# Performance work log

Hardware: AMD Instinct MI355X
Metric: run time of the kernel (lower is better)

The kernel has to match this reference:

```python
import jax, jax.numpy as jnp
import numpy as np

N_EMBD = 2048
QKV_EMBD = 2048
N_HEAD = 32
N_KV_HEAD = 8
HEAD_DIM = QKV_EMBD // N_HEAD  # 64
GROUPS = N_HEAD // N_KV_HEAD   # 4
ROPE_THETA = 10000.0
SCALE = float(np.sqrt(HEAD_DIM))


def setup_inputs() -> dict:
    key = jax.random.key(0)
    ks = jax.random.split(key, 12)
    B, S = 2, 2048
    inp = {
        "query": jax.random.normal(ks[0], (B, S, N_EMBD), jnp.float32),
        "key": jax.random.normal(ks[1], (B, S, N_EMBD), jnp.float32),
        "value": jax.random.normal(ks[2], (B, S, N_EMBD), jnp.float32),
        "mask": jnp.ones((B, S), dtype=bool),
        "Wq": jax.random.normal(ks[3], (QKV_EMBD, N_EMBD), jnp.float32) * 0.02,
        "bq": jnp.zeros((QKV_EMBD,), jnp.float32),
        "Wk": jax.random.normal(ks[4], (N_KV_HEAD * HEAD_DIM, N_EMBD), jnp.float32) * 0.02,
        "bk": jnp.zeros((N_KV_HEAD * HEAD_DIM,), jnp.float32),
        "Wv": jax.random.normal(ks[5], (N_KV_HEAD * HEAD_DIM, N_EMBD), jnp.float32) * 0.02,
        "bv": jnp.zeros((N_KV_HEAD * HEAD_DIM,), jnp.float32),
        "Wo": jax.random.normal(ks[6], (N_EMBD, QKV_EMBD), jnp.float32) * 0.02,
        "bo": jnp.zeros((N_EMBD,), jnp.float32),
    }
    return inp


def _rotate_half(x):
    d = x.shape[-1] // 2
    return jnp.concatenate([-x[..., d:], x[..., :d]], axis=-1)


def _rope_cos_sin(seq_len, dtype):
    # rope_factor == 1.0 -> no NTK adjustment; is_causal -> position_ids = arange
    inv_freq = 1.0 / (ROPE_THETA ** (jnp.arange(0, HEAD_DIM, 2, dtype=jnp.float32) / HEAD_DIM))
    pos = jnp.arange(seq_len, dtype=jnp.float32)
    freqs = jnp.einsum("i,j->ij", pos, inv_freq)           # [S, D/2]
    emb = jnp.concatenate([freqs, freqs], axis=-1)          # [S, D]
    return jnp.cos(emb).astype(dtype)[None, None], jnp.sin(emb).astype(dtype)[None, None]


def reference(query, key, value, mask, Wq, bq, Wk, bk, Wv, bv, Wo, bo):
    B, S, _ = query.shape
    Q = (query @ Wq.T + bq).reshape(B, S, N_HEAD, HEAD_DIM).transpose(0, 2, 1, 3)      # [B,H,S,D]
    K = (key @ Wk.T + bk).reshape(B, S, N_KV_HEAD, HEAD_DIM).transpose(0, 2, 1, 3)     # [B,KV,S,D]
    V = (value @ Wv.T + bv).reshape(B, S, N_KV_HEAD, HEAD_DIM).transpose(0, 2, 1, 3)

    cos, sin = _rope_cos_sin(S, Q.dtype)
    Q = Q * cos + _rotate_half(Q) * sin
    K = K * cos + _rotate_half(K) * sin

    # interleaved GQA repeat: each kv head serves GROUPS consecutive query heads
    K = jnp.repeat(K, GROUPS, axis=1)  # [B,H,S,D]
    V = jnp.repeat(V, GROUPS, axis=1)

    attn = jnp.einsum("bhqd,bhkd->bhqk", Q, K)              # [B,H,S,S]
    causal = jnp.tril(jnp.ones((S, S), dtype=bool))
    full_mask = mask[:, None, None, :] & causal[None, None]  # [B,1,S,S]
    attn = jnp.where(full_mask, attn, jnp.finfo(attn.dtype).min)
    attn_weights = jax.nn.softmax(attn / SCALE, axis=-1)     # dropout p=0 (eval)
    out = jnp.einsum("bhqk,bhkd->bhqd", attn_weights, V)
    out = out.transpose(0, 2, 1, 3).reshape(B, S, QKV_EMBD)
    return out @ Wo.T + bo
```

## Files before the change

kernel.cpp:

```cpp
#include <hip/hip_runtime.h>
#include <hip/hip_bf16.h>
#include <cmath>

#define NE   2048
#define NH   32
#define NKV  8
#define HD   64
#define SEQ  2048
#define NB   2

typedef __attribute__((ext_vector_type(4))) float f32x4;
typedef __attribute__((ext_vector_type(16))) float f32x16;
typedef __attribute__((ext_vector_type(8))) short bf16x8;
typedef __attribute__((ext_vector_type(4))) short bf16x4;
typedef __attribute__((ext_vector_type(4))) unsigned u32x4;

typedef const __attribute__((address_space(1))) void cgvoid;
typedef __attribute__((address_space(3))) void lvoid;

#define QSCALE 0.18033688011112042f

__device__ __forceinline__ short f2bf(float f) {
  union { float f; unsigned u; } v; v.f = f;
  unsigned r = v.u + 0x7fffu + ((v.u >> 16) & 1u);
  return (short)(r >> 16);
}

__device__ __forceinline__ unsigned cvt_pk_bf16(float a, float b) {
  unsigned r;
  asm("v_cvt_pk_bf16_f32 %0, %1, %2" : "=v"(r) : "v"(a), "v"(b));
  return r;
}

__global__ __launch_bounds__(256) void cvt_w(
    const float* __restrict__ s0, short* __restrict__ d0,
    const float* __restrict__ s1, short* __restrict__ d1,
    const float* __restrict__ s2, short* __restrict__ d2,
    const float* __restrict__ s3, short* __restrict__ d3)
{
  int idx = blockIdx.x * 256 + threadIdx.x;
  const float* s; short* d; int rel;
  if      (idx < 524288)  { s = s0; d = d0; rel = idx; }
  else if (idx < 655360)  { s = s1; d = d1; rel = idx - 524288; }
  else if (idx < 786432)  { s = s2; d = d2; rel = idx - 655360; }
  else                    { s = s3; d = d3; rel = idx - 786432; }
  size_t off = (size_t)rel * 8;
  f32x4 a = *(const f32x4*)(s + off);
  f32x4 b = *(const f32x4*)(s + off + 4);
  bf16x8 o;
  #pragma unroll
  for (int j = 0; j < 4; ++j) { o[j] = f2bf(a[j]); o[4 + j] = f2bf(b[j]); }
  *(bf16x8*)(d + off) = o;
}

template<int EPI>
__device__ __forceinline__ void gemm256_body(
    short* As, short* Ws, int m0, int n0,
    const float* __restrict__ A, const short* __restrict__ W,
    const float* __restrict__ bias, void* __restrict__ Cout, int K)
{
  const int t = threadIdx.x, lane = t & 63, w = t >> 6;
  const int lr = lane & 15, lg = lane >> 4;
  const int wm = (w >> 2) * 128, wn = (w & 3) * 64;

  f32x4 acc[8][4];
  #pragma unroll
  for (int i = 0; i < 8; ++i)
    #pragma unroll
    for (int j = 0; j < 4; ++j) acc[i][j] = (f32x4){0.f, 0.f, 0.f, 0.f};

  auto STAGE_W = [&](int kt) {
    const int k0 = kt << 6;
    short* Wd = Ws + (kt & 1) * 16384;
    #pragma unroll
    for (int it = 0; it < 4; ++it) {
      int e = it * 512 + t, r = e >> 3, c = e & 7;
      int cs = ((c ^ (r & 7)) << 3);
      __builtin_amdgcn_global_load_lds((cgvoid*)(W + (size_t)(n0 + r) * K + k0 + cs),
                                       (lvoid*)(Wd + e * 8), 16, 0, 0);
    }
  };

  f32x4 areg[4][2];
  auto LOAD_A = [&](int kt) {
    const int k0 = kt << 6;
    #pragma unroll
    for (int it = 0; it < 4; ++it) {
      int e = it * 512 + t, r = e >> 3, c = e & 7;
      int cs = ((c ^ (r & 7)) << 3);
      const float* src = A + (size_t)(m0 + r) * K + k0 + cs;
      areg[it][0] = *(const f32x4*)(src);
      areg[it][1] = *(const f32x4*)(src + 4);
    }
  };
  auto WRITE_A = [&](int kt) {
    short* Ad = As + (kt & 1) * 16384;
    #pragma unroll
    for (int it = 0; it < 4; ++it) {
      int e = it * 512 + t;
      u32x4 v;
      v[0] = cvt_pk_bf16(areg[it][0][0], areg[it][0][1]);
      v[1] = cvt_pk_bf16(areg[it][0][2], areg[it][0][3]);
      v[2] = cvt_pk_bf16(areg[it][1][0], areg[it][1][1]);
      v[3] = cvt_pk_bf16(areg[it][1][2], areg[it][1][3]);
      *(u32x4*)(Ad + e * 8) = v;
    }
  };

  const int nt = K >> 6;

  LOAD_A(0);
  STAGE_W(0);
  WRITE_A(0);
  asm volatile("s_waitcnt lgkmcnt(0)" ::: "memory");

  #pragma unroll 1
  for (int ti = 0; ti < nt; ++ti) {
    const short* Ab = As + (ti & 1) * 16384;
    const short* Wb = Ws + (ti & 1) * 16384;
    if (ti + 1 < nt) {
      LOAD_A(ti + 1);
      STAGE_W(ti + 1);
      asm volatile("s_waitcnt vmcnt(12)" ::: "memory");
    } else {
      asm volatile("s_waitcnt vmcnt(0)" ::: "memory");
    }
    __builtin_amdgcn_s_barrier();

    bf16x8 wf[2][4];
    #pragma unroll
    for (int ks = 0; ks < 2; ++ks)
      #pragma unroll
      for (int nf = 0; nf < 4; ++nf) {
        int row = wn + nf * 16 + lr;
        wf[ks][nf] = *(const bf16x8*)(Wb + row * 64 + (((ks * 4 + lg) ^ (row & 7)) << 3));
      }
    #pragma unroll
    for (int mq = 0; mq < 4; ++mq) {
      bf16x8 af[2][2];
      #pragma unroll
      for (int ks = 0; ks < 2; ++ks)
        #pragma unroll
        for (int mi = 0; mi < 2; ++mi) {
          int row = wm + (mq * 2 + mi) * 16 + lr;
          af[ks][mi] = *(const bf16x8*)(Ab + row * 64 + (((ks * 4 + lg) ^ (row & 7)) << 3));
        }
      __builtin_amdgcn_s_setprio(1);
      #pragma unroll
      for (int ks = 0; ks < 2; ++ks)
        #pragma unroll
        for (int mi = 0; mi < 2; ++mi)
          #pragma unroll
          for (int nf = 0; nf < 4; ++nf)
            acc[mq * 2 + mi][nf] =
                __builtin_amdgcn_mfma_f32_16x16x32_bf16(af[ks][mi], wf[ks][nf],
                                                        acc[mq * 2 + mi][nf], 0, 0, 0);
      __builtin_amdgcn_s_setprio(0);
    }
    if (ti + 1 < nt) WRITE_A(ti + 1);
    asm volatile("s_waitcnt lgkmcnt(0)" ::: "memory");
    __builtin_amdgcn_s_barrier();
  }

  if (EPI == 1) {
    short* C = (short*)Cout;
    #pragma unroll
    for (int mf = 0; mf < 8; ++mf)
      #pragma unroll
      for (int nf = 0; nf < 4; ++nf) {
        int n = n0 + wn + nf * 16 + lr;
        int kv = n >> 6, d = n & 63;
        int mb = m0 + wm + mf * 16 + lg * 4;
        int b = mb >> 11, s = mb & (SEQ - 1);
        bf16x4 pb;
        #pragma unroll
        for (int i = 0; i < 4; ++i) pb[i] = f2bf(acc[mf][nf][i] + bias[n]);
        *(bf16x4*)(C + (((size_t)b * NKV + kv) * HD + d) * SEQ + s) = pb;
      }
  } else {
    const int HN = (EPI == 2) ? NH : NKV;
    short* C = (short*)Cout;
    #pragma unroll
    for (int mf = 0; mf < 8; ++mf)
      #pragma unroll
      for (int nf2 = 0; nf2 < 2; ++nf2) {
        int n1 = n0 + wn + nf2 * 16 + lr;
        int d1 = n1 & 63;
        int h = n1 >> 6;
        float inv = exp2f(-(float)d1 * (13.287712379549449f / 32.0f));
        #pragma unroll
        for (int i = 0; i < 4; ++i) {
          int m = m0 + wm + mf * 16 + lg * 4 + i;
          int b = m >> 11, s = m & (SEQ - 1);
          float v1 = acc[mf][nf2][i] + bias[n1];
          float v2 = acc[mf][nf2 + 2][i] + bias[n1 + 32];
          float ang = (float)s * inv;
          float c, sn;
          __sincosf(ang, &sn, &c);
          float o1 = v1 * c - v2 * sn;
          float o2 = v2 * c + v1 * sn;
          if (EPI == 2) { o1 *= QSCALE; o2 *= QSCALE; }
          size_t base = (((size_t)b * HN + h) * SEQ + s) * HD;
          C[base + d1]      = f2bf(o1);
          C[base + d1 + 32] = f2bf(o2);
        }
      }
  }
}

__global__ __launch_bounds__(512, 2) void gemm_qkv256(
    const float* __restrict__ qA, const short* __restrict__ Wq,
    const float* __restrict__ bq, short* __restrict__ Qout,
    const float* __restrict__ kA, const short* __restrict__ Wk,
    const float* __restrict__ bk, short* __restrict__ Kout,
    const float* __restrict__ vA, const short* __restrict__ Wv,
    const float* __restrict__ bv, short* __restrict__ Vout)
{
  __shared__ __align__(16) short As[2 * 256 * 64];
  __shared__ __align__(16) short Ws[2 * 256 * 64];
  int orig = blockIdx.x;
  int xcd = orig & 7, idx = orig >> 3;
  int hiP = (idx >= 12) ? 1 : 0;
  int mm = xcd + 8 * hiP;
  int j = idx - 12 * hiP;
  if (j < 8) {
    gemm256_body<2>(As, Ws, mm * 256, j * 256, qA, Wq, bq, (void*)Qout, NE);
  } else if (j < 10) {
    gemm256_body<3>(As, Ws, mm * 256, (j - 8) * 256, kA, Wk, bk, (void*)Kout, NE);
  } else {
    gemm256_body<1>(As, Ws, mm * 256, (j - 10) * 256, vA, Wv, bv, (void*)Vout, NE);
  }
}

__global__ __launch_bounds__(256) void gemm_o(
    const short* __restrict__ A, const short* __restrict__ W,
    const float* __restrict__ bias, float* __restrict__ C, int N, int K)
{
  __shared__ __align__(16) short As[2 * 128 * 64];
  __shared__ __align__(16) short Ws[2 * 128 * 64];
  const int t = threadIdx.x, lane = t & 63, w = t >> 6;
  const int lr = lane & 15, lg = lane >> 4;
  const int wm = (w >> 1) * 64, wn = (w & 1) * 64;
  const int L = blockIdx.x;
  const int xcd = L & 7, slot = L >> 3;
  const int bx = xcd + 8 * (slot >> 4);
  const int byy = slot & 15;
  const int m0 = bx * 128, n0 = byy * 128;

  f32x4 acc[4][4];
  #pragma unroll
  for (int i = 0; i < 4; ++i)
    #pragma unroll
    for (int j = 0; j < 4; ++j) acc[i][j] = (f32x4){0.f, 0.f, 0.f, 0.f};

  const int nt = K >> 6;
  #pragma unroll
  for (int it = 0; it < 4; ++it) {
    int e = it * 256 + t, r = e >> 3, c = e & 7;
    int cs = ((c ^ (r & 7)) << 3);
    __builtin_amdgcn_global_load_lds((cgvoid*)(A + (size_t)(m0 + r) * K + cs),
                                     (lvoid*)(As + e * 8), 16, 0, 0);
    __builtin_amdgcn_global_load_lds((cgvoid*)(W + (size_t)(n0 + r) * K + cs),
                                     (lvoid*)(Ws + e * 8), 16, 0, 0);
  }

  for (int ti = 0; ti < nt; ++ti) {
    const int cur = ti & 1;
    const short* Ab = As + cur * 8192;
    const short* Wb = Ws + cur * 8192;
    if (ti + 1 < nt) {
      const int k0 = (ti + 1) << 6;
      short* An = As + (cur ^ 1) * 8192;
      short* Wn = Ws + (cur ^ 1) * 8192;
      #pragma unroll
      for (int it = 0; it < 4; ++it) {
        int e = it * 256 + t, r = e >> 3, c = e & 7;
        int cs = ((c ^ (r & 7)) << 3);
        __builtin_amdgcn_global_load_lds((cgvoid*)(A + (size_t)(m0 + r) * K + k0 + cs),
                                         (lvoid*)(An + e * 8), 16, 0, 0);
        __builtin_amdgcn_global_load_lds((cgvoid*)(W + (size_t)(n0 + r) * K + k0 + cs),
                                         (lvoid*)(Wn + e * 8), 16, 0, 0);
      }
      asm volatile("s_waitcnt vmcnt(8)" ::: "memory");
    } else {
      asm volatile("s_waitcnt vmcnt(0)" ::: "memory");
    }
    __builtin_amdgcn_s_barrier();
    __builtin_amdgcn_sched_barrier(0);

    bf16x8 wf[2][4];
    #pragma unroll
    for (int ks = 0; ks < 2; ++ks)
      #pragma unroll
      for (int nf = 0; nf < 4; ++nf) {
        int row = wn + nf * 16 + lr;
        wf[ks][nf] = *(const bf16x8*)(Wb + row * 64 + (((ks * 4 + lg) ^ (row & 7)) << 3));
      }
    #pragma unroll
    for (int mq = 0; mq < 2; ++mq) {
      bf16x8 af[2][2];
      #pragma unroll
      for (int ks = 0; ks < 2; ++ks)
        #pragma unroll
        for (int mi = 0; mi < 2; ++mi) {
          int row = wm + (mq * 2 + mi) * 16 + lr;
          af[ks][mi] = *(const bf16x8*)(Ab + row * 64 + (((ks * 4 + lg) ^ (row & 7)) << 3));
        }
      __builtin_amdgcn_s_setprio(1);
      #pragma unroll
      for (int ks = 0; ks < 2; ++ks)
        #pragma unroll
        for (int mi = 0; mi < 2; ++mi)
          #pragma unroll
          for (int nf = 0; nf < 4; ++nf)
            acc[mq * 2 + mi][nf] =
                __builtin_amdgcn_mfma_f32_16x16x32_bf16(af[ks][mi], wf[ks][nf],
                                                        acc[mq * 2 + mi][nf], 0, 0, 0);
      __builtin_amdgcn_s_setprio(0);
      __builtin_amdgcn_s_barrier();
      __builtin_amdgcn_sched_barrier(0);
    }
  }

  #pragma unroll
  for (int mf = 0; mf < 4; ++mf)
    #pragma unroll
    for (int nf = 0; nf < 4; ++nf)
      #pragma unroll
      for (int i = 0; i < 4; ++i) {
        int m = m0 + wm + mf * 16 + lg * 4 + i;
        int n = n0 + wn + nf * 16 + lr;
        C[(size_t)m * N + n] = acc[mf][nf][i] + bias[n];
      }
}

__global__ __launch_bounds__(256) void attn_kernel(
    const short* __restrict__ Q, const short* __restrict__ K,
    const short* __restrict__ Vt, short* __restrict__ O)
{
  __shared__ __align__(16) short Ks[2][64 * 64];
  __shared__ __align__(16) short Vs[2][64 * 64];

  const int t = threadIdx.x, lane = t & 63, w = t >> 6;
  const int l31 = lane & 31, hi = lane >> 5;
  const int L = blockIdx.x;
  const int xcd = L & 7, slot = L >> 3;
  const int by = xcd + 8 * (slot >> 5);
  const int bx = slot & 31;
  const int b = by >> 3, kvh = by & 7;
  const int h = kvh * 4 + w;

  const short* Qh = Q + ((size_t)b * NH + h) * SEQ * HD;
  const short* Kh = K + ((size_t)b * NKV + kvh) * SEQ * HD;
  const short* Vh = Vt + ((size_t)b * NKV + kvh) * (size_t)HD * SEQ;

  #pragma unroll 1
  for (int pass = 0; pass < 2; ++pass) {
    const int qb32 = pass ? bx : (63 - bx);
    const int q0 = qb32 * 32;
    const int ntile = (qb32 >> 1) + 1;
    const int qpos = q0 + l31;

    bf16x8 qfr[4];
    #pragma unroll
    for (int dd = 0; dd < 4; ++dd)
      qfr[dd] = *(const bf16x8*)(Qh + (size_t)(q0 + l31) * HD + dd * 16 + hi * 8);

    f32x16 o[2];
    #pragma unroll
    for (int dh = 0; dh < 2; ++dh)
      #pragma unroll
      for (int r = 0; r < 16; ++r) o[dh][r] = 0.f;
    float lsum = 0.f;

    #pragma unroll
    for (int it = 0; it < 2; ++it) {
      int cid = it * 256 + t;
      int r = cid >> 3, c = cid & 7;
      int cs = ((c ^ (r & 7)) << 3);
      __builtin_amdgcn_global_load_lds((cgvoid*)(Kh + (size_t)r * HD + cs),
                                       (lvoid*)(Ks[0] + cid * 8), 16, 0, 0);
      __builtin_amdgcn_global_load_lds((cgvoid*)(Vh + (size_t)r * SEQ + cs),
                                       (lvoid*)(Vs[0] + cid * 8), 16, 0, 0);
    }
    __syncthreads();

    for (int ti = 0; ti < ntile; ++ti) {
      const int cur = ti & 1;
      if (ti + 1 < ntile) {
        const int kvn = (ti + 1) * 64;
        #pragma unroll
        for (int it = 0; it < 2; ++it) {
          int cid = it * 256 + t;
          int r = cid >> 3, c = cid & 7;
          int cs = ((c ^ (r & 7)) << 3);
          __builtin_amdgcn_global_load_lds((cgvoid*)(Kh + (size_t)(kvn + r) * HD + cs),
                                           (lvoid*)(Ks[cur ^ 1] + cid * 8), 16, 0, 0);
          __builtin_amdgcn_global_load_lds((cgvoid*)(Vh + (size_t)r * SEQ + kvn + cs),
                                           (lvoid*)(Vs[cur ^ 1] + cid * 8), 16, 0, 0);
        }
      }
      const int kv0 = ti * 64;
      const short* Kb = Ks[cur];
      const short* Vb = Vs[cur];

      f32x16 p[2];
      __builtin_amdgcn_s_setprio(1);
      #pragma unroll
      for (int f = 0; f < 2; ++f) {
        f32x16 z;
        #pragma unroll
        for (int r = 0; r < 16; ++r) z[r] = 0.f;
        #pragma unroll
        for (int dd = 0; dd < 4; ++dd) {
          int row = f * 32 + l31;
          bf16x8 ka = *(const bf16x8*)(Kb + row * 64 + (((2 * dd + hi) ^ (row & 7)) << 3));
          z = __builtin_amdgcn_mfma_f32_32x32x16_bf16(ka, qfr[dd], z, 0, 0, 0);
        }
        p[f] = z;
      }
      __builtin_amdgcn_s_setprio(0);

      if (ti == ntile - 1) {
        #pragma unroll
        for (int f = 0; f < 2; ++f)
          #pragma unroll
          for (int r = 0; r < 16; ++r) {
            int kpos = kv0 + f * 32 + (r & 3) + 8 * (r >> 2) + 4 * hi;
            if (kpos > qpos) p[f][r] = -INFINITY;
          }
      }

      unsigned pa[4][4];
      #pragma unroll
      for (int f = 0; f < 2; ++f) {
        float e[16];
        #pragma unroll
        for (int r = 0; r < 16; ++r) {
          e[r] = __builtin_amdgcn_exp2f(p[f][r]);
          lsum += e[r];
        }
        unsigned c[8];
        #pragma unroll
        for (int i = 0; i < 8; ++i) c[i] = cvt_pk_bf16(e[2 * i], e[2 * i + 1]);
        asm volatile("v_permlane32_swap_b32 %0, %1" : "+v"(c[0]), "+v"(c[2]));
        asm volatile("v_permlane32_swap_b32 %0, %1" : "+v"(c[1]), "+v"(c[3]));
        asm volatile("v_permlane32_swap_b32 %0, %1" : "+v"(c[4]), "+v"(c[6]));
        asm volatile("v_permlane32_swap_b32 %0, %1" : "+v"(c[5]), "+v"(c[7]));
        pa[2 * f][0] = c[0]; pa[2 * f][1] = c[1]; pa[2 * f][2] = c[2]; pa[2 * f][3] = c[3];
        pa[2 * f + 1][0] = c[4]; pa[2 * f + 1][1] = c[5];
        pa[2 * f + 1][2] = c[6]; pa[2 * f + 1][3] = c[7];
      }

      __builtin_amdgcn_s_setprio(1);
      #pragma unroll
      for (int ks = 0; ks < 4; ++ks) {
        bf16x8 paf = *(const bf16x8*)&pa[ks][0];
        #pragma unroll
        for (int dh = 0; dh < 2; ++dh) {
          int row = dh * 32 + l31;
          bf16x8 vb = *(const bf16x8*)(Vb + row * 64 + (((2 * ks + hi) ^ (row & 7)) << 3));
          o[dh] = __builtin_amdgcn_mfma_f32_32x32x16_bf16(paf, vb, o[dh], 0, 0, 0);
        }
      }
      __builtin_amdgcn_s_setprio(0);
      __syncthreads();
    }

    lsum += __shfl_xor(lsum, 32);
    #pragma unroll
    for (int r = 0; r < 16; ++r) {
      int crow = (r & 3) + 8 * (r >> 2) + 4 * hi;
      float li = __shfl(lsum, crow, 64);
      float invl = 1.0f / li;
      int s = q0 + crow;
      size_t base = (((size_t)b * SEQ + s) * NH + h) * HD;
      O[base + l31]      = f2bf(o[0][r] * invl);
      O[base + 32 + l31] = f2bf(o[1][r] * invl);
    }
  }
}

extern "C" void kernel_launch(void* const* d_in, const int* in_sizes, int n_in,
                              void* d_out, int out_size, void* d_ws, size_t ws_size,
                              hipStream_t stream) {
  (void)in_sizes; (void)n_in; (void)out_size; (void)ws_size;
  const float* q  = (const float*)d_in[0];
  const float* k  = (const float*)d_in[1];
  const float* v  = (const float*)d_in[2];
  const float* Wq = (const float*)d_in[4];
  const float* bq = (const float*)d_in[5];
  const float* Wk = (const float*)d_in[6];
  const float* bk = (const float*)d_in[7];
  const float* Wv = (const float*)d_in[8];
  const float* bv = (const float*)d_in[9];
  const float* Wo = (const float*)d_in[10];
  const float* bo = (const float*)d_in[11];

  const size_t SQ2 = (size_t)NB * SEQ * NE;
  const size_t W1  = (size_t)NE * NE;
  const size_t W2  = (size_t)(NKV * HD) * NE;
  const size_t KVN = (size_t)NB * NKV * SEQ * HD;

  short* ws = (short*)d_ws;
  short* Wqb = ws;
  short* Wkb = Wqb + W1;
  short* Wvb = Wkb + W2;
  short* Wob = Wvb + W2;
  short* Qr  = Wob + W1;
  short* Kr  = Qr + SQ2;
  short* Vr  = Kr + KVN;
  short* Ob  = Vr + KVN;

  dim3 blk(256);

  cvt_w<<<5120, blk, 0, stream>>>(Wq, Wqb, Wk, Wkb, Wv, Wvb, Wo, Wob);
  gemm_qkv256<<<192, dim3(512), 0, stream>>>(q, Wqb, bq, Qr, k, Wkb, bk, Kr, v, Wvb, bv, Vr);
  attn_kernel<<<512, blk, 0, stream>>>(Qr, Kr, Vr, Ob);
  gemm_o<<<512, blk, 0, stream>>>(Ob, Wob, bo, (float*)d_out, NE, NE);
}
```

Before: 191.3 us.

## Enlarge output projection GEMM to 256x256 tiles with 512-thread blocks

The output projection GEMM moves from 128x128 tiles with 256 threads (512 blocks) to 256x256 tiles with 512 threads (128 blocks), mirroring the QKV GEMM. Each wave now computes a 128x64 sub-tile, raising operand reuse per LDS load and cutting global traffic. The per-mq barriers inside the k-step are removed, leaving one barrier at the end of each k-step. With only 128 blocks on a 256-CU device, half the CUs may sit idle, and the larger accumulator raises register pressure.

```diff
diff --git a/kernel.cpp b/kernel.cpp
--- a/kernel.cpp
+++ b/kernel.cpp
@@ -232,61 +232,59 @@
   }
 }
 
-__global__ __launch_bounds__(256) void gemm_o(
+__global__ __launch_bounds__(512, 2) void gemm_o256(
     const short* __restrict__ A, const short* __restrict__ W,
-    const float* __restrict__ bias, float* __restrict__ C, int N, int K)
+    const float* __restrict__ bias, float* __restrict__ C)
 {
-  __shared__ __align__(16) short As[2 * 128 * 64];
-  __shared__ __align__(16) short Ws[2 * 128 * 64];
+  __shared__ __align__(16) short As[2 * 256 * 64];
+  __shared__ __align__(16) short Ws[2 * 256 * 64];
+  const int K = NE, N = NE;
+
+  int orig = blockIdx.x;
+  int xcd = orig & 7, idx = orig >> 3;
+  int mm = xcd + 8 * (idx >> 3);
+  int j = idx & 7;
+  const int m0 = mm * 256, n0 = j * 256;
+
   const int t = threadIdx.x, lane = t & 63, w = t >> 6;
   const int lr = lane & 15, lg = lane >> 4;
-  const int wm = (w >> 1) * 64, wn = (w & 1) * 64;
-  const int L = blockIdx.x;
-  const int xcd = L & 7, slot = L >> 3;
-  const int bx = xcd + 8 * (slot >> 4);
-  const int byy = slot & 15;
-  const int m0 = bx * 128, n0 = byy * 128;
-
-  f32x4 acc[4][4];
+  const int wm = (w >> 2) * 128, wn = (w & 3) * 64;
+
+  f32x4 acc[8][4];
   #pragma unroll
-  for (int i = 0; i < 4; ++i)
-    #pragma unroll
-    for (int j = 0; j < 4; ++j) acc[i][j] = (f32x4){0.f, 0.f, 0.f, 0.f};
+  for (int i = 0; i < 8; ++i)
+    #pragma unroll
+    for (int jj = 0; jj < 4; ++jj) acc[i][jj] = (f32x4){0.f, 0.f, 0.f, 0.f};
+
+  auto STAGE = [&](int kt) {
+    const int k0 = kt << 6;
+    short* Ad = As + (kt & 1) * 16384;
+    short* Wd = Ws + (kt & 1) * 16384;
+    #pragma unroll
+    for (int it = 0; it < 4; ++it) {
+      int e = it * 512 + t, r = e >> 3, c = e & 7;
+      int cs = ((c ^ (r & 7)) << 3);
+      __builtin_amdgcn_global_load_lds((cgvoid*)(A + (size_t)(m0 + r) * K + k0 + cs),
+                                       (lvoid*)(Ad + e * 8), 16, 0, 0);
+      __builtin_amdgcn_global_load_lds((cgvoid*)(W + (size_t)(n0 + r) * K + k0 + cs),
+                                       (lvoid*)(Wd + e * 8), 16, 0, 0);
+    }
+  };
 
   const int nt = K >> 6;
-  #pragma unroll
-  for (int it = 0; it < 4; ++it) {
-    int e = it * 256 + t, r = e >> 3, c = e & 7;
-    int cs = ((c ^ (r & 7)) << 3);
-    __builtin_amdgcn_global_load_lds((cgvoid*)(A + (size_t)(m0 + r) * K + cs),
-                                     (lvoid*)(As + e * 8), 16, 0, 0);
-    __builtin_amdgcn_global_load_lds((cgvoid*)(W + (size_t)(n0 + r) * K + cs),
-                                     (lvoid*)(Ws + e * 8), 16, 0, 0);
-  }
-
+  STAGE(0);
+
+  #pragma unroll 1
   for (int ti = 0; ti < nt; ++ti) {
-    const int cur = ti & 1;
-    const short* Ab = As + cur * 8192;
-    const short* Wb = Ws + cur * 8192;
+    const short* Ab = As + (ti & 1) * 16384;
+    const short* Wb = Ws + (ti & 1) * 16384;
     if (ti + 1 < nt) {
-      const int k0 = (ti + 1) << 6;
-      short* An = As + (cur ^ 1) * 8192;
-      short* Wn = Ws + (cur ^ 1) * 8192;
-      #pragma unroll
-      for (int it = 0; it < 4; ++it) {
-        int e = it * 256 + t, r = e >> 3, c = e & 7;
-        int cs = ((c ^ (r & 7)) << 3);
-        __builtin_amdgcn_global_load_lds((cgvoid*)(A + (size_t)(m0 + r) * K + k0 + cs),
-                                         (lvoid*)(An + e * 8), 16, 0, 0);
-        __builtin_amdgcn_global_load_lds((cgvoid*)(W + (size_t)(n0 + r) * K + k0 + cs),
-                                         (lvoid*)(Wn + e * 8), 16, 0, 0);
-      }
+      STAGE(ti + 1);
       asm volatile("s_waitcnt vmcnt(8)" ::: "memory");
     } else {
       asm volatile("s_waitcnt vmcnt(0)" ::: "memory");
     }
     __builtin_amdgcn_s_barrier();
-    __builtin_amdgcn_sched_barrier(0);
 
     bf16x8 wf[2][4];
     #pragma unroll
@@ -297,7 +295,7 @@
         wf[ks][nf] = *(const bf16x8*)(Wb + row * 64 + (((ks * 4 + lg) ^ (row & 7)) << 3));
       }
     #pragma unroll
-    for (int mq = 0; mq < 2; ++mq) {
+    for (int mq = 0; mq < 4; ++mq) {
       bf16x8 af[2][2];
       #pragma unroll
       for (int ks = 0; ks < 2; ++ks)
@@ -317,21 +315,22 @@
                 __builtin_amdgcn_mfma_f32_16x16x32_bf16(af[ks][mi], wf[ks][nf],
                                                         acc[mq * 2 + mi][nf], 0, 0, 0);
       __builtin_amdgcn_s_setprio(0);
-      __builtin_amdgcn_s_barrier();
-      __builtin_amdgcn_sched_barrier(0);
-    }
+    }
+    __builtin_amdgcn_s_barrier();
   }
 
   #pragma unroll
-  for (int mf = 0; mf < 4; ++mf)
-    #pragma unroll
-    for (int nf = 0; nf < 4; ++nf)
+  for (int mf = 0; mf < 8; ++mf)
+    #pragma unroll
+    for (int nf = 0; nf < 4; ++nf) {
+      int n = n0 + wn + nf * 16 + lr;
+      float bn = bias[n];
       #pragma unroll
       for (int i = 0; i < 4; ++i) {
         int m = m0 + wm + mf * 16 + lg * 4 + i;
-        int n = n0 + wn + nf * 16 + lr;
-        C[(size_t)m * N + n] = acc[mf][nf][i] + bias[n];
-      }
+        C[(size_t)m * N + n] = acc[mf][nf][i] + bn;
+      }
+    }
 }
 
 __global__ __launch_bounds__(256) void attn_kernel(
@@ -517,5 +516,5 @@
   cvt_w<<<5120, blk, 0, stream>>>(Wq, Wqb, Wk, Wkb, Wv, Wvb, Wo, Wob);
   gemm_qkv256<<<192, dim3(512), 0, stream>>>(q, Wqb, bq, Qr, k, Wkb, bk, Kr, v, Wvb, bv, Vr);
   attn_kernel<<<512, blk, 0, stream>>>(Qr, Kr, Vr, Ob);
-  gemm_o<<<512, blk, 0, stream>>>(Ob, Wob, bo, (float*)d_out, NE, NE);
-}
+  gemm_o256<<<128, dim3(512), 0, stream>>>(Ob, Wob, bo, (float*)d_out);
+}
```

Result: slower. 215.6 us (+12.7%).
